# Kernel tuning notes

Hardware: AMD Instinct MI355X
Metric: run time of the kernel (lower is better)

Reference implementation:

```python
import jax, jax.numpy as jnp
import numpy as np

NUM_CLASSES = 3
IMG = 448
STRIDES = (8, 16, 32)
POS_IOU, NEG_IOU = 0.5, 0.3
NEG_RATIO = 3
B, T = 64, 20


def _make_anchors(stride):
    f = IMG // stride
    cs = (np.arange(f, dtype=np.float32) + 0.5) * stride
    cx, cy = np.meshgrid(cs, cs, indexing='xy')            # [f, f]
    sizes = np.array([2.0, 2.5, 3.0], np.float32) * stride  # 3 square anchors / loc
    cx = np.broadcast_to(cx[..., None], (f, f, 3))
    cy = np.broadcast_to(cy[..., None], (f, f, 3))
    w = np.broadcast_to(sizes, (f, f, 3))
    boxes = np.stack([cx - w / 2, cy - w / 2, cx + w / 2, cy + w / 2], -1)
    return jnp.asarray(boxes.reshape(-1, 4), jnp.float32)   # [f*f*3, 4]


def setup_inputs() -> dict:
    key = jax.random.key(0)
    k1, k2, k3, kc, ks, kl = jax.random.split(key, 6)
    pred1 = jax.random.normal(k1, (B, 24, 56, 56), jnp.float32)
    pred2 = jax.random.normal(k2, (B, 24, 28, 28), jnp.float32)
    pred3 = jax.random.normal(k3, (B, 24, 14, 14), jnp.float32)
    ctr = jax.random.uniform(kc, (B, T, 2), jnp.float32, 20.0, IMG - 20.0)
    wh = jax.random.uniform(ks, (B, T, 2), jnp.float32, 20.0, 120.0)
    target_boxes = jnp.concatenate([ctr - wh / 2, ctr + wh / 2], axis=-1)  # [B,T,4] xyxy
    target_labels = jax.random.randint(kl, (B, T), 1, NUM_CLASSES + 1, jnp.int32)
    return {
        'pred1': pred1, 'pred2': pred2, 'pred3': pred3,
        'anchor1': _make_anchors(8), 'anchor2': _make_anchors(16), 'anchor3': _make_anchors(32),
        'target_boxes': target_boxes, 'target_labels': target_labels,
    }


def _iou(a, b):  # a [A,4], b [T,4] -> [A,T]
    lt = jnp.maximum(a[:, None, :2], b[None, :, :2])
    rb = jnp.minimum(a[:, None, 2:], b[None, :, 2:])
    wh = jnp.clip(rb - lt, 0.0)
    inter = wh[..., 0] * wh[..., 1]
    area_a = (a[:, 2] - a[:, 0]) * (a[:, 3] - a[:, 1])
    area_b = (b[:, 2] - b[:, 0]) * (b[:, 3] - b[:, 1])
    return inter / (area_a[:, None] + area_b[None, :] - inter + 1e-9)


def _encode(gt, an):  # both [A,4] xyxy -> [A,4] deltas
    aw, ah = an[:, 2] - an[:, 0], an[:, 3] - an[:, 1]
    acx, acy = (an[:, 0] + an[:, 2]) * 0.5, (an[:, 1] + an[:, 3]) * 0.5
    gw, gh = gt[:, 2] - gt[:, 0], gt[:, 3] - gt[:, 1]
    gcx, gcy = (gt[:, 0] + gt[:, 2]) * 0.5, (gt[:, 1] + gt[:, 3]) * 0.5
    return jnp.stack([(gcx - acx) / aw, (gcy - acy) / ah,
                      jnp.log(gw / aw), jnp.log(gh / ah)], axis=-1)


def _bce_logits(x, y):
    return jnp.maximum(x, 0.0) - x * y + jnp.log1p(jnp.exp(-jnp.abs(x)))


def _image_loss(deltas, obj, cls, boxes, labels, anchors):
    # deltas [A,4], obj [A], cls [A,K], boxes [T,4], labels [T], anchors [A,4]
    iou = _iou(anchors, boxes)                    # [A,T]
    matched_t = jnp.argmax(iou, axis=1)           # [A]
    max_iou = jnp.max(iou, axis=1)
    pos = max_iou >= POS_IOU
    neg = max_iou < NEG_IOU
    # force each GT's best anchor to be positive
    best_a = jnp.argmax(iou, axis=0)              # [T]
    matched_t = matched_t.at[best_a].set(jnp.arange(boxes.shape[0]))
    pos = pos.at[best_a].set(True)
    neg = neg.at[best_a].set(False)
    matched_labels = jnp.where(pos, labels[matched_t], 0)
    # objectness + hard negative mining (rank-based topk, jit-safe)
    obj_t = (matched_labels > 0).astype(obj.dtype)
    bce = _bce_logits(obj, obj_t)
    num_pos = pos.sum()
    need = jnp.minimum(NEG_RATIO * num_pos, neg.sum())
    rank = jnp.argsort(jnp.argsort(-jnp.where(neg, bce, -jnp.inf)))
    sel = pos | ((rank < need) & neg)
    obj_loss = jnp.sum(jnp.where(sel, bce, 0.0)) / jnp.maximum(sel.sum(), 1)
    # classification (mean over positives)
    logp = jax.nn.log_softmax(cls, axis=-1)
    tgt = jnp.maximum(matched_labels - 1, 0)
    ce = -jnp.take_along_axis(logp, tgt[:, None], axis=1)[:, 0]
    cls_loss = jnp.sum(jnp.where(pos, ce, 0.0)) / jnp.maximum(num_pos, 1)
    # localization: smooth L1, mean over positive anchor elements
    tdel = _encode(boxes[matched_t], anchors)
    d = jnp.abs(deltas - tdel)
    sl1 = jnp.where(d < 1.0, 0.5 * d * d, d - 0.5)
    loc_loss = jnp.sum(jnp.where(pos[:, None], sl1, 0.0)) / jnp.maximum(4 * num_pos, 1)
    return obj_loss, cls_loss, loc_loss


def _scale_loss(pred, anchors, boxes, labels):
    Bp, C, H, W = pred.shape
    p = pred.transpose(0, 2, 3, 1).reshape(Bp, H * W * 3, 5 + NUM_CLASSES)
    deltas, obj, cls = p[..., :4], p[..., 4], p[..., 5:]
    fn = jax.vmap(lambda d, o, c, b, l: _image_loss(d, o, c, b, l, anchors))
    ol, cl, ll = fn(deltas, obj, cls, boxes, labels)
    return ol.sum(), cl.sum(), ll.sum()


def reference(pred1, pred2, pred3, anchor1, anchor2, anchor3, target_boxes, target_labels):
    tot = jnp.zeros(3, jnp.float32)
    for pred, anc in ((pred1, anchor1), (pred2, anchor2), (pred3, anchor3)):
        ol, cl, ll = _scale_loss(pred, anc, target_boxes, target_labels)
        tot = tot + jnp.stack([ol, cl, ll])
    bsz = target_boxes.shape[0]
    obj, cls, loc = tot[0] / bsz, tot[1] / bsz, tot[2] / bsz
    total = obj + cls + 2.0 * loc
    return jnp.stack([obj, cls, loc, total])
```

## Files before the change

kernel.cpp:

```cpp
#include <hip/hip_runtime.h>
#include <math.h>

#define T 20
#define MAXA 9408
#define APB 12348
#define LOSS_OFF 16
#define KEY_OFF  2048
#define MF_BYTE_OFF (4 * (KEY_OFF + 64 * APB))

static __device__ __forceinline__ unsigned mapf(float x) {
    unsigned u = __float_as_uint(x);
    return (u & 0x80000000u) ? ~u : (u | 0x80000000u);
}
static __device__ __forceinline__ float unmapf(unsigned m) {
    return __uint_as_float((m & 0x80000000u) ? (m ^ 0x80000000u) : ~m);
}
static __device__ __forceinline__ float bce_pos(float x) {
    return fmaxf(x, 0.f) - x + log1pf(expf(-fabsf(x)));
}
static __device__ __forceinline__ float bce_neg(float x) {
    return fmaxf(x, 0.f) + log1pf(expf(-fabsf(x)));
}

__global__ __launch_bounds__(256) void match_kernel(
    const float* __restrict__ pred1, const float* __restrict__ pred2,
    const float* __restrict__ pred3, const float* __restrict__ tboxes,
    unsigned* __restrict__ wsu, unsigned short* __restrict__ mf)
{
#pragma clang fp contract(off)
    const int blk = blockIdx.x;
    const int b = blk / 11, c = blk - 11 * b;
    int s, j0;
    if (c < 8)       { s = 0; j0 = c * 1176; }
    else if (c < 10) { s = 1; j0 = (c - 8) * 1176; }
    else             { s = 2; j0 = 0; }
    const float* __restrict__ pred = (s == 0) ? pred1 : (s == 1) ? pred2 : pred3;
    const int W = 56 >> s, HW = W * W, A = 3 * HW;
    const float stf = (float)(8 << s);
    const int sh = 3 - s;
    const int lim = min(1176, A - j0);

    __shared__ float4 s_box[T];
    __shared__ float  s_ab[T];
    const int tid = threadIdx.x;

    if (tid < T) {
        float4 g = ((const float4*)tboxes)[b * T + tid];
        s_box[tid] = g;
        s_ab[tid]  = (g.z - g.x) * (g.w - g.y);
    }
    __syncthreads();

    float ax[5], ay[5], az[5], aw[5], ar[5], bn[5], bu[5];
    int at_[5], kk[5], pp[5];
    bool vv[5];
    float xlo = 1e30f, xhi = -1e30f, ylo = 1e30f, yhi = -1e30f;
    const int obase = 5 * tid;
#pragma unroll
    for (int r = 0; r < 5; r++) {
        int o = obase + r;
        vv[r] = (o < lim);
        int j = j0 + (vv[r] ? o : 0);
        int k   = (j >= HW) + (j >= 2 * HW);
        int pix = j - k * HW;
        int qq  = pix >> sh;
        int py  = (qq * 9363) >> 16;
        int px  = pix - py * W;
        float w  = (2.0f + 0.5f * (float)k) * stf;
        float cx = ((float)px + 0.5f) * stf;
        float cy = ((float)py + 0.5f) * stf;
        ax[r] = cx - 0.5f * w; ay[r] = cy - 0.5f * w;
        az[r] = cx + 0.5f * w; aw[r] = cy + 0.5f * w;
        ar[r] = w * w;
        bn[r] = 0.f; bu[r] = 1.f; at_[r] = 0;
        kk[r] = k; pp[r] = pix;
        xlo = fminf(xlo, ax[r]); xhi = fmaxf(xhi, az[r]);
        ylo = fminf(ylo, ay[r]); yhi = fmaxf(yhi, aw[r]);
    }

    for (int t = 0; t < T; t++) {
        float4 g = s_box[t];
        if (g.x < xhi && g.z > xlo && g.y < yhi && g.w > ylo) {
            float ab = s_ab[t];
#pragma unroll
            for (int r = 0; r < 5; r++) {
                float lx = fmaxf(ax[r], g.x), ly = fmaxf(ay[r], g.y);
                float rx = fminf(az[r], g.z), ry = fminf(aw[r], g.w);
                float ww = fmaxf(rx - lx, 0.f), hh = fmaxf(ry - ly, 0.f);
                float inter = ww * hh;
                float u = ((ar[r] + ab) - inter) + 1e-9f;
                if (inter * bu[r] > bn[r] * u) { bn[r] = inter; bu[r] = u; at_[r] = t; }
            }
        }
    }

    const float* objbase = pred + (size_t)(b * 24 + 4) * HW;
    const unsigned base = (unsigned)(b * APB + ((s == 0) ? 0 : (s == 1) ? 9408 : 11760));
#pragma unroll
    for (int r = 0; r < 5; r++) {
        if (vv[r]) {
            int j = j0 + obase + r;
            bool pos = (bn[r] + bn[r] >= bu[r]);
            bool neg = (bn[r] < 0.3f * bu[r]);
            unsigned key = 0u;
            if (neg) key = mapf(objbase[(size_t)kk[r] * 8 * HW + pp[r]]);
            wsu[KEY_OFF + base + j] = key;
            mf[base + j] = (unsigned short)(at_[r] | (pos ? 0x100 : 0) | (neg ? 0x200 : 0));
        }
    }
}

__global__ __launch_bounds__(512) void select_loss_kernel(
    const float* __restrict__ pred1, const float* __restrict__ pred2,
    const float* __restrict__ pred3, const float* __restrict__ tboxes,
    const int* __restrict__ tlabels,
    const unsigned* __restrict__ wsu, const unsigned short* __restrict__ mf,
    float* __restrict__ wsf)
{
#pragma clang fp contract(off)
    const int bid = blockIdx.x;
    const int b = bid / 3, s = bid - 3 * b;
    const float* __restrict__ pred = (s == 0) ? pred1 : (s == 1) ? pred2 : pred3;
    const int W = 56 >> s, HW = W * W, A = 3 * HW;
    const float stf = (float)(8 << s);
    const int sh = 3 - s;
    const unsigned base = (unsigned)(b * APB + ((s == 0) ? 0 : (s == 1) ? 9408 : 11760));

    __shared__ unsigned       s_key[MAXA];
    __shared__ unsigned short s_mf[MAXA];
    __shared__ float4   s_box[T];
    __shared__ float    s_ab[T];
    __shared__ int      s_lab[T];
    __shared__ int      s_besta[T];
    __shared__ unsigned whist[4][256];
    __shared__ unsigned s_npnn;
    __shared__ unsigned s_bc[2];
    __shared__ float    s_redf[8 * 4];

    const int tid = threadIdx.x, lane = tid & 63, wid = tid >> 6;

    if (tid < T) {
        float4 g = ((const float4*)tboxes)[b * T + tid];
        s_box[tid] = g;
        s_ab[tid]  = (g.z - g.x) * (g.w - g.y);
        s_lab[tid] = tlabels[b * T + tid];
    }
    if (tid == 0) s_npnn = 0u;
    __syncthreads();

    for (int j = tid; j < A; j += 512) {
        s_key[j] = wsu[KEY_OFF + base + j];
        s_mf[j]  = mf[base + j];
    }

    for (int t = wid; t < T; t += 8) {
        float4 g = s_box[t];
        float  ab = s_ab[t];
        int px0 = max(0, (int)floorf(g.x / stf) - 2);
        int px1 = min(W - 1, (int)floorf(g.z / stf) + 2);
        int py0 = max(0, (int)floorf(g.y / stf) - 2);
        int py1 = min(W - 1, (int)floorf(g.w / stf) + 2);
        int rowlen = (px1 - px0 + 1) * 3;
        float bi = -1.f, bu2 = 1.f;
        int ba = 0;
        for (int py = py0; py <= py1; py++) {
            float cy = ((float)py + 0.5f) * stf;
            for (int cc = lane; cc < rowlen; cc += 64) {
                int ix = (cc * 21846) >> 16;
                int k  = cc - 3 * ix;
                int px = px0 + ix;
                float w  = (2.0f + 0.5f * (float)k) * stf;
                float cx = ((float)px + 0.5f) * stf;
                float lx = fmaxf(cx - 0.5f * w, g.x), ly = fmaxf(cy - 0.5f * w, g.y);
                float rx = fminf(cx + 0.5f * w, g.z), ry = fminf(cy + 0.5f * w, g.w);
                float ww = fmaxf(rx - lx, 0.f), hh = fmaxf(ry - ly, 0.f);
                float inter = ww * hh;
                float u = ((w * w + ab) - inter) + 1e-9f;
                if (inter * bu2 > bi * u) {
                    bi = inter; bu2 = u; ba = (py * W + px) * 3 + k;
                }
            }
        }
        for (int off = 32; off; off >>= 1) {
            float oi = __shfl_down(bi, off, 64);
            float ou = __shfl_down(bu2, off, 64);
            int   oa = __shfl_down(ba, off, 64);
            float l = oi * bu2, r = bi * ou;
            if (l > r || (l == r && oa < ba)) { bi = oi; bu2 = ou; ba = oa; }
        }
        if (lane == 0) {
            int pix = (ba * 21846) >> 16;
            int k = ba - 3 * pix;
            s_besta[t] = k * HW + pix;
        }
    }
    __syncthreads();

    if (tid < T) {
        int j20 = s_besta[tid];
        bool winner = true;
        for (int t2 = tid + 1; t2 < T; t2++) if (s_besta[t2] == j20) winner = false;
        if (winner) {
            s_mf[j20]  = (unsigned short)(tid | 0x100);
            s_key[j20] = 0u;
        }
    }
    __syncthreads();

    unsigned npnn = 0;
    for (int j = tid; j < A; j += 512) {
        unsigned m = s_mf[j];
        npnn += ((m >> 8) & 1u) + (((m >> 9) & 1u) << 16);
    }
    for (int off = 32; off; off >>= 1) npnn += (unsigned)__shfl_down((int)npnn, off, 64);
    if (lane == 0) atomicAdd(&s_npnn, npnn);
    __syncthreads();
    unsigned np = s_npnn & 0xFFFFu, nn = s_npnn >> 16;
    unsigned need = min(3u * np, nn);

    unsigned kth = 0xFFFFFFFFu;
    if (need > 0) {
        unsigned prefix = 0, remaining = need;
        for (int p = 0; p < 4; p++) {
            const int sh_ = 24 - 8 * p;
            if (tid < 256) {
                whist[0][tid] = 0; whist[1][tid] = 0;
                whist[2][tid] = 0; whist[3][tid] = 0;
            }
            __syncthreads();
            for (int j = tid; j < A; j += 512) {
                unsigned k = s_key[j];
                bool ok = (p == 0) || ((k >> (sh_ + 8)) == prefix);
                if (ok) atomicAdd(&whist[wid >> 1][(k >> sh_) & 255u], 1u);
            }
            __syncthreads();
            if (tid < 256) {
                whist[0][tid] = whist[0][tid] + whist[1][tid]
                              + whist[2][tid] + whist[3][tid];
            }
            __syncthreads();
            if (wid == 0) {
                int b0 = lane * 4;
                unsigned csum = whist[0][b0] + whist[0][b0 + 1]
                              + whist[0][b0 + 2] + whist[0][b0 + 3];
                unsigned Tv = csum;
                for (int off = 1; off < 64; off <<= 1) {
                    unsigned o = __shfl_down(Tv, off, 64);
                    if (lane + off < 64) Tv += o;
                }
                unsigned long long ball = __ballot(Tv >= remaining);
                int L = 63 - __clzll(ball);
                if (lane == L) {
                    unsigned sv = Tv - csum;
                    int bb = b0 + 3;
                    while (true) { sv += whist[0][bb]; if (sv >= remaining) break; bb--; }
                    s_bc[0] = (unsigned)bb;
                    s_bc[1] = sv - whist[0][bb];
                }
            }
            __syncthreads();
            remaining -= s_bc[1];
            prefix = (prefix << 8) | s_bc[0];
        }
        kth = prefix;
    }

    float obj_s = 0.f, cls_s = 0.f, loc_s = 0.f;
    unsigned cgt = 0;
    for (int j = tid; j < A; j += 512) {
        unsigned mfv = s_mf[j];
        if (mfv & 0x100u) {
            int k   = (j >= HW) + (j >= 2 * HW);
            int pix = j - k * HW;
            const float* bp = pred + (size_t)(b * 24 + k * 8) * HW + pix;
            float x = bp[(size_t)4 * HW];
            obj_s += bce_pos(x);
            int t = mfv & 0xFFu;
            float4 g = s_box[t];
            int tgt = s_lab[t] - 1;
            float c0 = bp[(size_t)5 * HW], c1 = bp[(size_t)6 * HW], c2 = bp[(size_t)7 * HW];
            float mm  = fmaxf(c0, fmaxf(c1, c2));
            float lse = logf(expf(c0 - mm) + expf(c1 - mm) + expf(c2 - mm));
            float ct = (tgt == 0) ? c0 : (tgt == 1) ? c1 : c2;
            cls_s += (mm + lse) - ct;
            int qq = pix >> sh;
            int py = (qq * 9363) >> 16;
            int px = pix - py * W;
            float w  = (2.0f + 0.5f * (float)k) * stf;
            float cx = ((float)px + 0.5f) * stf;
            float cy = ((float)py + 0.5f) * stf;
            float gcx = (g.x + g.z) * 0.5f, gcy = (g.y + g.w) * 0.5f;
            float gw = g.z - g.x, gh = g.w - g.y;
            float t0 = (gcx - cx) / w, t1 = (gcy - cy) / w;
            float t2 = logf(gw / w),   t3 = logf(gh / w);
            float d0 = bp[0], d1 = bp[(size_t)HW], d2 = bp[(size_t)2 * HW], d3 = bp[(size_t)3 * HW];
            float dd;
            dd = fabsf(d0 - t0); loc_s += (dd < 1.f) ? 0.5f * dd * dd : dd - 0.5f;
            dd = fabsf(d1 - t1); loc_s += (dd < 1.f) ? 0.5f * dd * dd : dd - 0.5f;
            dd = fabsf(d2 - t2); loc_s += (dd < 1.f) ? 0.5f * dd * dd : dd - 0.5f;
            dd = fabsf(d3 - t3); loc_s += (dd < 1.f) ? 0.5f * dd * dd : dd - 0.5f;
        } else {
            unsigned key = s_key[j];
            if (key > kth) { obj_s += bce_neg(unmapf(key)); cgt++; }
        }
    }
    for (int off = 32; off; off >>= 1) {
        obj_s += __shfl_down(obj_s, off, 64);
        cls_s += __shfl_down(cls_s, off, 64);
        loc_s += __shfl_down(loc_s, off, 64);
        cgt   += (unsigned)__shfl_down((int)cgt, off, 64);
    }
    if (lane == 0) {
        s_redf[wid * 4 + 0] = obj_s;
        s_redf[wid * 4 + 1] = cls_s;
        s_redf[wid * 4 + 2] = loc_s;
        s_redf[wid * 4 + 3] = __uint_as_float(cgt);
    }
    __syncthreads();
    if (tid == 0) {
        float ob = 0.f, cl = 0.f, lc = 0.f;
        unsigned cg = 0;
        for (int w2 = 0; w2 < 8; w2++) {
            ob += s_redf[w2 * 4 + 0];
            cl += s_redf[w2 * 4 + 1];
            lc += s_redf[w2 * 4 + 2];
            cg += __float_as_uint(s_redf[w2 * 4 + 3]);
        }
        if (need > 0) ob += (float)(need - cg) * bce_neg(unmapf(kth));
        wsf[LOSS_OFF + bid * 3 + 0] = ob / (float)max(np + need, 1u);
        wsf[LOSS_OFF + bid * 3 + 1] = cl / (float)max(np, 1u);
        wsf[LOSS_OFF + bid * 3 + 2] = lc / (float)max(4u * np, 1u);
    }
}

__global__ void finalize_kernel(const float* __restrict__ wsf,
                                float* __restrict__ out) {
    const int t = threadIdx.x, lane = t & 63, wid = t >> 6;
    __shared__ float red[12];
    float v0 = 0.f, v1 = 0.f, v2 = 0.f;
    if (t < 192) {
        v0 = wsf[LOSS_OFF + 3 * t];
        v1 = wsf[LOSS_OFF + 3 * t + 1];
        v2 = wsf[LOSS_OFF + 3 * t + 2];
    }
    for (int off = 32; off; off >>= 1) {
        v0 += __shfl_down(v0, off, 64);
        v1 += __shfl_down(v1, off, 64);
        v2 += __shfl_down(v2, off, 64);
    }
    if (lane == 0) { red[wid * 3] = v0; red[wid * 3 + 1] = v1; red[wid * 3 + 2] = v2; }
    __syncthreads();
    if (t == 0) {
        float obj = 0.f, cls = 0.f, loc = 0.f;
        for (int w2 = 0; w2 < 4; w2++) {
            obj += red[w2 * 3]; cls += red[w2 * 3 + 1]; loc += red[w2 * 3 + 2];
        }
        obj /= 64.f; cls /= 64.f; loc /= 64.f;
        out[0] = obj; out[1] = cls; out[2] = loc;
        out[3] = obj + cls + 2.f * loc;
    }
}

extern "C" void kernel_launch(void* const* d_in, const int* in_sizes, int n_in,
                              void* d_out, int out_size, void* d_ws, size_t ws_size,
                              hipStream_t stream) {
    const float* pred1   = (const float*)d_in[0];
    const float* pred2   = (const float*)d_in[1];
    const float* pred3   = (const float*)d_in[2];
    const float* tboxes  = (const float*)d_in[6];
    const int*   tlabels = (const int*)d_in[7];
    unsigned* wsu = (unsigned*)d_ws;
    unsigned short* mf = (unsigned short*)((char*)d_ws + MF_BYTE_OFF);
    float* wsf = (float*)d_ws;
    float* out = (float*)d_out;

    match_kernel<<<64 * 11, 256, 0, stream>>>(pred1, pred2, pred3, tboxes, wsu, mf);
    select_loss_kernel<<<64 * 3, 512, 0, stream>>>(
        pred1, pred2, pred3, tboxes, tlabels, wsu, mf, wsf);
    finalize_kernel<<<1, 256, 0, stream>>>(wsf, out);
}
```

Before: 135.1 us.

## Fuse anchor matching into select-loss kernel, keep keys in shared memory

```diff
diff --git a/kernel.cpp b/kernel.cpp
--- a/kernel.cpp
+++ b/kernel.cpp
@@ -3,10 +3,7 @@
 
 #define T 20
 #define MAXA 9408
-#define APB 12348
 #define LOSS_OFF 16
-#define KEY_OFF  2048
-#define MF_BYTE_OFF (4 * (KEY_OFF + 64 * APB))
 
 static __device__ __forceinline__ unsigned mapf(float x) {
     unsigned u = __float_as_uint(x);
@@ -22,100 +19,10 @@
     return fmaxf(x, 0.f) + log1pf(expf(-fabsf(x)));
 }
 
-__global__ __launch_bounds__(256) void match_kernel(
+__global__ __launch_bounds__(1024, 1) void fused_kernel(
     const float* __restrict__ pred1, const float* __restrict__ pred2,
     const float* __restrict__ pred3, const float* __restrict__ tboxes,
-    unsigned* __restrict__ wsu, unsigned short* __restrict__ mf)
-{
-#pragma clang fp contract(off)
-    const int blk = blockIdx.x;
-    const int b = blk / 11, c = blk - 11 * b;
-    int s, j0;
-    if (c < 8)       { s = 0; j0 = c * 1176; }
-    else if (c < 10) { s = 1; j0 = (c - 8) * 1176; }
-    else             { s = 2; j0 = 0; }
-    const float* __restrict__ pred = (s == 0) ? pred1 : (s == 1) ? pred2 : pred3;
-    const int W = 56 >> s, HW = W * W, A = 3 * HW;
-    const float stf = (float)(8 << s);
-    const int sh = 3 - s;
-    const int lim = min(1176, A - j0);
-
-    __shared__ float4 s_box[T];
-    __shared__ float  s_ab[T];
-    const int tid = threadIdx.x;
-
-    if (tid < T) {
-        float4 g = ((const float4*)tboxes)[b * T + tid];
-        s_box[tid] = g;
-        s_ab[tid]  = (g.z - g.x) * (g.w - g.y);
-    }
-    __syncthreads();
-
-    float ax[5], ay[5], az[5], aw[5], ar[5], bn[5], bu[5];
-    int at_[5], kk[5], pp[5];
-    bool vv[5];
-    float xlo = 1e30f, xhi = -1e30f, ylo = 1e30f, yhi = -1e30f;
-    const int obase = 5 * tid;
-#pragma unroll
-    for (int r = 0; r < 5; r++) {
-        int o = obase + r;
-        vv[r] = (o < lim);
-        int j = j0 + (vv[r] ? o : 0);
-        int k   = (j >= HW) + (j >= 2 * HW);
-        int pix = j - k * HW;
-        int qq  = pix >> sh;
-        int py  = (qq * 9363) >> 16;
-        int px  = pix - py * W;
-        float w  = (2.0f + 0.5f * (float)k) * stf;
-        float cx = ((float)px + 0.5f) * stf;
-        float cy = ((float)py + 0.5f) * stf;
-        ax[r] = cx - 0.5f * w; ay[r] = cy - 0.5f * w;
-        az[r] = cx + 0.5f * w; aw[r] = cy + 0.5f * w;
-        ar[r] = w * w;
-        bn[r] = 0.f; bu[r] = 1.f; at_[r] = 0;
-        kk[r] = k; pp[r] = pix;
-        xlo = fminf(xlo, ax[r]); xhi = fmaxf(xhi, az[r]);
-        ylo = fminf(ylo, ay[r]); yhi = fmaxf(yhi, aw[r]);
-    }
-
-    for (int t = 0; t < T; t++) {
-        float4 g = s_box[t];
-        if (g.x < xhi && g.z > xlo && g.y < yhi && g.w > ylo) {
-            float ab = s_ab[t];
-#pragma unroll
-            for (int r = 0; r < 5; r++) {
-                float lx = fmaxf(ax[r], g.x), ly = fmaxf(ay[r], g.y);
-                float rx = fminf(az[r], g.z), ry = fminf(aw[r], g.w);
-                float ww = fmaxf(rx - lx, 0.f), hh = fmaxf(ry - ly, 0.f);
-                float inter = ww * hh;
-                float u = ((ar[r] + ab) - inter) + 1e-9f;
-                if (inter * bu[r] > bn[r] * u) { bn[r] = inter; bu[r] = u; at_[r] = t; }
-            }
-        }
-    }
-
-    const float* objbase = pred + (size_t)(b * 24 + 4) * HW;
-    const unsigned base = (unsigned)(b * APB + ((s == 0) ? 0 : (s == 1) ? 9408 : 11760));
-#pragma unroll
-    for (int r = 0; r < 5; r++) {
-        if (vv[r]) {
-            int j = j0 + obase + r;
-            bool pos = (bn[r] + bn[r] >= bu[r]);
-            bool neg = (bn[r] < 0.3f * bu[r]);
-            unsigned key = 0u;
-            if (neg) key = mapf(objbase[(size_t)kk[r] * 8 * HW + pp[r]]);
-            wsu[KEY_OFF + base + j] = key;
-            mf[base + j] = (unsigned short)(at_[r] | (pos ? 0x100 : 0) | (neg ? 0x200 : 0));
-        }
-    }
-}
-
-__global__ __launch_bounds__(512) void select_loss_kernel(
-    const float* __restrict__ pred1, const float* __restrict__ pred2,
-    const float* __restrict__ pred3, const float* __restrict__ tboxes,
-    const int* __restrict__ tlabels,
-    const unsigned* __restrict__ wsu, const unsigned short* __restrict__ mf,
-    float* __restrict__ wsf)
+    const int* __restrict__ tlabels, float* __restrict__ wsf)
 {
 #pragma clang fp contract(off)
     const int bid = blockIdx.x;
@@ -124,7 +31,6 @@
     const int W = 56 >> s, HW = W * W, A = 3 * HW;
     const float stf = (float)(8 << s);
     const int sh = 3 - s;
-    const unsigned base = (unsigned)(b * APB + ((s == 0) ? 0 : (s == 1) ? 9408 : 11760));
 
     __shared__ unsigned       s_key[MAXA];
     __shared__ unsigned short s_mf[MAXA];
@@ -135,7 +41,7 @@
     __shared__ unsigned whist[4][256];
     __shared__ unsigned s_npnn;
     __shared__ unsigned s_bc[2];
-    __shared__ float    s_redf[8 * 4];
+    __shared__ float    s_redf[16 * 4];
 
     const int tid = threadIdx.x, lane = tid & 63, wid = tid >> 6;
 
@@ -148,12 +54,62 @@
     if (tid == 0) s_npnn = 0u;
     __syncthreads();
 
-    for (int j = tid; j < A; j += 512) {
-        s_key[j] = wsu[KEY_OFF + base + j];
-        s_mf[j]  = mf[base + j];
-    }
-
-    for (int t = wid; t < T; t += 8) {
+    const float* objbase = pred + (size_t)(b * 24 + 4) * HW;
+
+    for (int j0 = 4 * tid; j0 < A; j0 += 4096) {
+        float ax[4], ay[4], az[4], aw[4], ar[4], bn[4], bu[4];
+        int at_[4];
+        float xlo = 1e30f, xhi = -1e30f, ylo = 1e30f, yhi = -1e30f;
+#pragma unroll
+        for (int r = 0; r < 4; r++) {
+            int j = j0 + r;
+            int k   = (j >= HW) + (j >= 2 * HW);
+            int pix = j - k * HW;
+            int qq  = pix >> sh;
+            int py  = (qq * 9363) >> 16;
+            int px  = pix - py * W;
+            float w  = (2.0f + 0.5f * (float)k) * stf;
+            float cx = ((float)px + 0.5f) * stf;
+            float cy = ((float)py + 0.5f) * stf;
+            ax[r] = cx - 0.5f * w; ay[r] = cy - 0.5f * w;
+            az[r] = cx + 0.5f * w; aw[r] = cy + 0.5f * w;
+            ar[r] = w * w;
+            bn[r] = 0.f; bu[r] = 1.f; at_[r] = 0;
+            xlo = fminf(xlo, ax[r]); xhi = fmaxf(xhi, az[r]);
+            ylo = fminf(ylo, ay[r]); yhi = fmaxf(yhi, aw[r]);
+        }
+        for (int t = 0; t < T; t++) {
+            float4 g = s_box[t];
+            if (g.x < xhi && g.z > xlo && g.y < yhi && g.w > ylo) {
+                float ab = s_ab[t];
+#pragma unroll
+                for (int r = 0; r < 4; r++) {
+                    float lx = fmaxf(ax[r], g.x), ly = fmaxf(ay[r], g.y);
+                    float rx = fminf(az[r], g.z), ry = fminf(aw[r], g.w);
+                    float ww = fmaxf(rx - lx, 0.f), hh = fmaxf(ry - ly, 0.f);
+                    float inter = ww * hh;
+                    float u = ((ar[r] + ab) - inter) + 1e-9f;
+                    if (inter * bu[r] > bn[r] * u) {
+                        bn[r] = inter; bu[r] = u; at_[r] = t;
+                    }
+                }
+            }
+        }
+#pragma unroll
+        for (int r = 0; r < 4; r++) {
+            int j = j0 + r;
+            int k   = (j >= HW) + (j >= 2 * HW);
+            int pix = j - k * HW;
+            bool pos = (bn[r] + bn[r] >= bu[r]);
+            bool neg = (bn[r] < 0.3f * bu[r]);
+            unsigned key = 0u;
+            if (neg) key = mapf(objbase[(size_t)k * 8 * HW + pix]);
+            s_key[j] = key;
+            s_mf[j]  = (unsigned short)(at_[r] | (pos ? 0x100 : 0) | (neg ? 0x200 : 0));
+        }
+    }
+
+    for (int t = wid; t < T; t += 16) {
         float4 g = s_box[t];
         float  ab = s_ab[t];
         int px0 = max(0, (int)floorf(g.x / stf) - 2);
@@ -208,7 +164,7 @@
     __syncthreads();
 
     unsigned npnn = 0;
-    for (int j = tid; j < A; j += 512) {
+    for (int j = tid; j < A; j += 1024) {
         unsigned m = s_mf[j];
         npnn += ((m >> 8) & 1u) + (((m >> 9) & 1u) << 16);
     }
@@ -223,15 +179,12 @@
         unsigned prefix = 0, remaining = need;
         for (int p = 0; p < 4; p++) {
             const int sh_ = 24 - 8 * p;
-            if (tid < 256) {
-                whist[0][tid] = 0; whist[1][tid] = 0;
-                whist[2][tid] = 0; whist[3][tid] = 0;
-            }
-            __syncthreads();
-            for (int j = tid; j < A; j += 512) {
+            (&whist[0][0])[tid] = 0u;
+            __syncthreads();
+            for (int j = tid; j < A; j += 1024) {
                 unsigned k = s_key[j];
                 bool ok = (p == 0) || ((k >> (sh_ + 8)) == prefix);
-                if (ok) atomicAdd(&whist[wid >> 1][(k >> sh_) & 255u], 1u);
+                if (ok) atomicAdd(&whist[wid >> 2][(k >> sh_) & 255u], 1u);
             }
             __syncthreads();
             if (tid < 256) {
@@ -261,13 +214,14 @@
             __syncthreads();
             remaining -= s_bc[1];
             prefix = (prefix << 8) | s_bc[0];
+            __syncthreads();
         }
         kth = prefix;
     }
 
     float obj_s = 0.f, cls_s = 0.f, loc_s = 0.f;
     unsigned cgt = 0;
-    for (int j = tid; j < A; j += 512) {
+    for (int j = tid; j < A; j += 1024) {
         unsigned mfv = s_mf[j];
         if (mfv & 0x100u) {
             int k   = (j >= HW) + (j >= 2 * HW);
@@ -320,7 +274,7 @@
     if (tid == 0) {
         float ob = 0.f, cl = 0.f, lc = 0.f;
         unsigned cg = 0;
-        for (int w2 = 0; w2 < 8; w2++) {
+        for (int w2 = 0; w2 < 16; w2++) {
             ob += s_redf[w2 * 4 + 0];
             cl += s_redf[w2 * 4 + 1];
             lc += s_redf[w2 * 4 + 2];
@@ -369,13 +323,10 @@
     const float* pred3   = (const float*)d_in[2];
     const float* tboxes  = (const float*)d_in[6];
     const int*   tlabels = (const int*)d_in[7];
-    unsigned* wsu = (unsigned*)d_ws;
-    unsigned short* mf = (unsigned short*)((char*)d_ws + MF_BYTE_OFF);
     float* wsf = (float*)d_ws;
     float* out = (float*)d_out;
 
-    match_kernel<<<64 * 11, 256, 0, stream>>>(pred1, pred2, pred3, tboxes, wsu, mf);
-    select_loss_kernel<<<64 * 3, 512, 0, stream>>>(
-        pred1, pred2, pred3, tboxes, tlabels, wsu, mf, wsf);
+    fused_kernel<<<64 * 3, 1024, 0, stream>>>(
+        pred1, pred2, pred3, tboxes, tlabels, wsf);
     finalize_kernel<<<1, 256, 0, stream>>>(wsf, out);
 }
```

After: 116.9 us. 13.5% less time.
